# Optimization experiments

Measured on AMD Instinct MI355X. Metric: run time of the kernel, lower is better.

Reference implementation:

```python
import jax, jax.numpy as jnp
import numpy as np

H, C = 4, 32          # heads, per-head channels (hidden=128)
NEG_SLOPE = 0.2        # PyG GATv2Conv default LeakyReLU slope


def setup_inputs() -> dict:
    key = jax.random.key(0)
    ks = jax.random.split(key, 9)
    N_a, N_m = 100000, 50000     # asset / market node counts
    E_aa, E_am = 600000, 400000  # edge counts per edge type
    D, L = 128, 2                # hidden dims, num GAT layers
    sc = 1.0 / np.sqrt(D).astype(np.float32)

    x_asset = jax.random.normal(ks[0], (N_a, D), jnp.float32)
    x_market = jax.random.normal(ks[1], (N_m, D), jnp.float32)

    edge_aa = jax.random.randint(ks[2], (2, E_aa), 0, N_a, jnp.int32)
    src_am = jax.random.randint(ks[3], (E_am,), 0, N_a, jnp.int32)
    dst_am = jax.random.randint(ks[4], (E_am,), 0, N_m, jnp.int32)
    edge_am = jnp.stack([src_am, dst_am])

    Wl = jax.random.normal(ks[5], (L, D, D), jnp.float32) * sc   # lin_l (src)
    Wr = jax.random.normal(ks[6], (L, D, D), jnp.float32) * sc   # lin_r (dst)
    att = jax.random.normal(ks[7], (L, H, C), jnp.float32) * sc  # attention vector
    bias = jnp.zeros((L, D), jnp.float32)

    return {"x_asset": x_asset, "x_market": x_market,
            "edge_aa": edge_aa, "edge_am": edge_am,
            "Wl": Wl, "Wr": Wr, "att": att, "bias": bias}


def _gatv2(x_src, x_dst, src, dst, Wl, Wr, att, bias):
    """One GATv2Conv: gather-attend-scatter. x_src:[Ns,D], x_dst:[Nd,D]."""
    N_dst = x_dst.shape[0]
    xl = (x_src @ Wl).reshape(-1, H, C)   # transformed src (messages)
    xr = (x_dst @ Wr).reshape(-1, H, C)   # transformed dst
    z = jax.nn.leaky_relu(xl[src] + xr[dst], NEG_SLOPE)     # [E,H,C]
    e = jnp.einsum('ehc,hc->eh', z, att)                    # [E,H] scores
    # softmax over incoming edges per destination node
    m = jax.lax.stop_gradient(jax.ops.segment_max(e, dst, num_segments=N_dst))
    w = jnp.exp(e - m[dst])
    s = jax.ops.segment_sum(w, dst, num_segments=N_dst)
    alpha = w / jnp.maximum(s[dst], jnp.float32(1e-16))     # [E,H]
    out = jax.ops.segment_sum(alpha[..., None] * xl[src], dst, num_segments=N_dst)
    return out.reshape(N_dst, H * C) + bias


def reference(x_asset, x_market, edge_aa, edge_am, Wl, Wr, att, bias):
    # Faithful to source: x_dict is never updated between layers, so every
    # layer reads the ORIGINAL features and only the last layer's dict is kept.
    L = Wl.shape[0]
    out_asset = out_market = None
    for l in range(L):
        out_asset = _gatv2(x_asset, x_asset, edge_aa[0], edge_aa[1],
                           Wl[l], Wr[l], att[l], bias[l])
        out_market = _gatv2(x_asset, x_market, edge_am[0], edge_am[1],
                            Wl[l], Wr[l], att[l], bias[l])
    return out_asset, out_market
```

## Files before the change

kernel.cpp:

```cpp
#include <hip/hip_runtime.h>
#include <hip/hip_bf16.h>


#define NEG_SLOPE 0.2f

typedef __attribute__((ext_vector_type(8))) short short8;
typedef __attribute__((ext_vector_type(4))) float floatx4;
typedef __attribute__((ext_vector_type(4))) unsigned short us4;

__device__ inline unsigned short f2bf(float x) {
    union { float f; unsigned u; } v; v.f = x;
    unsigned r = v.u + 0x7FFF + ((v.u >> 16) & 1);
    return (unsigned short)(r >> 16);
}
__device__ inline float bf2f(unsigned short h) {
    union { unsigned u; float f; } v; v.u = (unsigned)h << 16;
    return v.f;
}

__device__ inline void stage_w(const float* __restrict__ W, unsigned char* lds, int t) {
    const int n = t & 127;
    const int kh = t >> 7;
    unsigned short hb[32], lb[32];
#pragma unroll
    for (int i = 0; i < 32; ++i) {
        int k = kh * 32 + i;
        float w = W[(size_t)k * 128 + n];
        unsigned short h = f2bf(w);
        hb[i] = h;
        lb[i] = f2bf(w - bf2f(h));
    }
#pragma unroll
    for (int j = 0; j < 4; ++j) {
        int k = kh * 32 + j * 8;
        int off = ((n * 256 + k * 2) ^ ((n & 7) << 4));
        short8 hv, lv;
#pragma unroll
        for (int i = 0; i < 8; ++i) { hv[i] = (short)hb[j * 8 + i]; lv[i] = (short)lb[j * 8 + i]; }
        *(short8*)(&lds[off]) = hv;
        *(short8*)(&lds[32768 + off]) = lv;
    }
}

__device__ inline void mfma_pass(const unsigned char* lds, const short8* ah,
                                 const short8* al, int lr, int lkb, floatx4* acc) {
#pragma unroll
    for (int ks = 0; ks < 4; ++ks) {
#pragma unroll
        for (int ct = 0; ct < 8; ++ct) {
            int n = ct * 16 + lr;
            int off = ((n * 256 + (ks * 32 + lkb) * 2) ^ ((n & 7) << 4));
            short8 bh = *(const short8*)(&lds[off]);
            short8 bl = *(const short8*)(&lds[32768 + off]);
            acc[ct] = __builtin_amdgcn_mfma_f32_16x16x32_bf16(ah[ks], bh, acc[ct], 0, 0, 0);
            acc[ct] = __builtin_amdgcn_mfma_f32_16x16x32_bf16(al[ks], bh, acc[ct], 0, 0, 0);
            acc[ct] = __builtin_amdgcn_mfma_f32_16x16x32_bf16(ah[ks], bl, acc[ct], 0, 0, 0);
        }
    }
}

__global__ __launch_bounds__(512) void gemm_all(const float* __restrict__ Xa,
                                                const float* __restrict__ Xm,
                                                const float* __restrict__ Wl,
                                                const float* __restrict__ Wr,
                                                unsigned short* __restrict__ XLb,
                                                float* __restrict__ XR,
                                                int Na, int Nm, int nblkA) {
    __shared__ __align__(16) unsigned char lds[65536];

    const int t = threadIdx.x;
    const int wv = t >> 6;
    const int l = t & 63;
    const int lr = l & 15;
    const int lkb = (l >> 4) * 8;
    const bool isA = ((int)blockIdx.x < nblkA);
    const int blk = isA ? blockIdx.x : blockIdx.x - nblkA;
    const float* __restrict__ X = isA ? Xa : Xm;
    const int M = isA ? Na : Nm;
    const int arow = blk * 128 + wv * 16 + lr;

    short8 ah[4], al[4];
    if (arow < M) {
#pragma unroll
        for (int ks = 0; ks < 4; ++ks) {
            const float* xp = X + (size_t)arow * 128 + ks * 32 + lkb;
            float4 f0 = *(const float4*)xp;
            float4 f1 = *(const float4*)(xp + 4);
            float xv[8] = {f0.x, f0.y, f0.z, f0.w, f1.x, f1.y, f1.z, f1.w};
            short8 h, lo;
#pragma unroll
            for (int i = 0; i < 8; ++i) {
                unsigned short hb = f2bf(xv[i]);
                h[i] = (short)hb;
                lo[i] = (short)f2bf(xv[i] - bf2f(hb));
            }
            ah[ks] = h; al[ks] = lo;
        }
    } else {
#pragma unroll
        for (int ks = 0; ks < 4; ++ks) { ah[ks] = (short8)0; al[ks] = (short8)0; }
    }

    const int orow0 = blk * 128 + wv * 16 + (l >> 4) * 4;
    floatx4 acc[8];

    if (isA) {
        stage_w(Wl, lds, t);
        __syncthreads();
#pragma unroll
        for (int ct = 0; ct < 8; ++ct) acc[ct] = (floatx4)0.f;
        mfma_pass(lds, ah, al, lr, lkb, acc);
#pragma unroll
        for (int ct = 0; ct < 8; ++ct) {
            int col = ct * 16 + lr;
#pragma unroll
            for (int r = 0; r < 4; ++r) {
                int orow = orow0 + r;
                if (orow < M) XLb[(size_t)orow * 128 + col] = f2bf(acc[ct][r]);
            }
        }
        __syncthreads();
        stage_w(Wr, lds, t);
        __syncthreads();
#pragma unroll
        for (int ct = 0; ct < 8; ++ct) acc[ct] = (floatx4)0.f;
        mfma_pass(lds, ah, al, lr, lkb, acc);
#pragma unroll
        for (int ct = 0; ct < 8; ++ct) {
            int col = ct * 16 + lr;
#pragma unroll
            for (int r = 0; r < 4; ++r) {
                int orow = orow0 + r;
                if (orow < M) XR[(size_t)orow * 128 + col] = acc[ct][r];
            }
        }
    } else {
        stage_w(Wr, lds, t);
        __syncthreads();
#pragma unroll
        for (int ct = 0; ct < 8; ++ct) acc[ct] = (floatx4)0.f;
        mfma_pass(lds, ah, al, lr, lkb, acc);
        float* __restrict__ XRm = XR + (size_t)Na * 128;
#pragma unroll
        for (int ct = 0; ct < 8; ++ct) {
            int col = ct * 16 + lr;
#pragma unroll
            for (int r = 0; r < 4; ++r) {
                int orow = orow0 + r;
                if (orow < M) XRm[(size_t)orow * 128 + col] = acc[ct][r];
            }
        }
    }
}

__global__ void degcount(const int* __restrict__ aadst, const int* __restrict__ amdst,
                         int* __restrict__ deg, int Eaa, int Eam, int Na) {
    const int nqaa = Eaa >> 2, nqam = Eam >> 2;
    int i = blockIdx.x * 256 + threadIdx.x;
    if (i < nqaa) {
        int4 d = ((const int4*)aadst)[i];
        atomicAdd(&deg[d.x], 1); atomicAdd(&deg[d.y], 1);
        atomicAdd(&deg[d.z], 1); atomicAdd(&deg[d.w], 1);
    } else if (i < nqaa + nqam) {
        int4 d = ((const int4*)amdst)[i - nqaa];
        atomicAdd(&deg[Na + d.x], 1); atomicAdd(&deg[Na + d.y], 1);
        atomicAdd(&deg[Na + d.z], 1); atomicAdd(&deg[Na + d.w], 1);
    } else {
        int k = i - (nqaa + nqam);
        int remaa = Eaa & 3, remam = Eam & 3;
        if (k < remaa) atomicAdd(&deg[aadst[nqaa * 4 + k]], 1);
        else if (k - remaa < remam) atomicAdd(&deg[Na + amdst[nqam * 4 + k - remaa]], 1);
    }
}

__global__ void scan_bsum(const int* __restrict__ deg, int* __restrict__ bsum, int N) {
    __shared__ int sd[256];
    int t = threadIdx.x;
    int base = blockIdx.x * 1024 + t * 4;
    int s = 0;
#pragma unroll
    for (int q = 0; q < 4; ++q) { int idx = base + q; if (idx < N) s += deg[idx]; }
    sd[t] = s; __syncthreads();
    for (int off = 128; off > 0; off >>= 1) {
        if (t < off) sd[t] += sd[t + off];
        __syncthreads();
    }
    if (t == 0) bsum[blockIdx.x] = sd[0];
}

__global__ void scan_partials(int* __restrict__ bsum, int nblk) {
    __shared__ int sd[256];
    int t = threadIdx.x;
    int v = (t < nblk) ? bsum[t] : 0;
    sd[t] = v; __syncthreads();
    for (int off = 1; off < 256; off <<= 1) {
        int x = sd[t];
        if (t >= off) x += sd[t - off];
        __syncthreads(); sd[t] = x; __syncthreads();
    }
    if (t < nblk) bsum[t] = (t == 0) ? 0 : sd[t - 1];
    if (t == 0) bsum[nblk] = sd[255];
}

__global__ void scan_final(const int* __restrict__ deg, const int* __restrict__ bsum,
                           int* __restrict__ row_start, int* __restrict__ fill,
                           int N, int nblk) {
    __shared__ int sd[256];
    int t = threadIdx.x;
    int base = blockIdx.x * 1024 + t * 4;
    int v[4]; int s = 0;
#pragma unroll
    for (int q = 0; q < 4; ++q) { int idx = base + q; v[q] = (idx < N) ? deg[idx] : 0; s += v[q]; }
    sd[t] = s; __syncthreads();
    for (int off = 1; off < 256; off <<= 1) {
        int x = sd[t];
        if (t >= off) x += sd[t - off];
        __syncthreads(); sd[t] = x; __syncthreads();
    }
    int run = bsum[blockIdx.x] + ((t == 0) ? 0 : sd[t - 1]);
#pragma unroll
    for (int q = 0; q < 4; ++q) {
        int idx = base + q;
        if (idx < N) { row_start[idx] = run; fill[idx] = run; }
        run += v[q];
    }
    if (blockIdx.x == 0 && t == 0) row_start[N] = bsum[nblk];
}

__global__ void fillcsr(const int* __restrict__ aasrc, const int* __restrict__ aadst,
                        const int* __restrict__ amsrc, const int* __restrict__ amdst,
                        int* __restrict__ fill, int* __restrict__ csr,
                        int Eaa, int Eam, int Na) {
    const int nqaa = Eaa >> 2, nqam = Eam >> 2;
    int i = blockIdx.x * 256 + threadIdx.x;
    if (i < nqaa) {
        int4 sv = ((const int4*)aasrc)[i];
        int4 dv = ((const int4*)aadst)[i];
        csr[atomicAdd(&fill[dv.x], 1)] = sv.x;
        csr[atomicAdd(&fill[dv.y], 1)] = sv.y;
        csr[atomicAdd(&fill[dv.z], 1)] = sv.z;
        csr[atomicAdd(&fill[dv.w], 1)] = sv.w;
    } else if (i < nqaa + nqam) {
        int4 sv = ((const int4*)amsrc)[i - nqaa];
        int4 dv = ((const int4*)amdst)[i - nqaa];
        csr[atomicAdd(&fill[Na + dv.x], 1)] = sv.x;
        csr[atomicAdd(&fill[Na + dv.y], 1)] = sv.y;
        csr[atomicAdd(&fill[Na + dv.z], 1)] = sv.z;
        csr[atomicAdd(&fill[Na + dv.w], 1)] = sv.w;
    } else {
        int k = i - (nqaa + nqam);
        int remaa = Eaa & 3, remam = Eam & 3;
        if (k < remaa)
            csr[atomicAdd(&fill[aadst[nqaa * 4 + k]], 1)] = aasrc[nqaa * 4 + k];
        else if (k - remaa < remam)
            csr[atomicAdd(&fill[Na + amdst[nqam * 4 + k - remaa]], 1)] = amsrc[nqam * 4 + k - remaa];
    }
}

__global__ __launch_bounds__(256) void gather_gat(const unsigned short* __restrict__ XLb,
                                                  const int* __restrict__ csr,
                                                  const int* __restrict__ row_start,
                                                  const float* __restrict__ att,
                                                  const float* __restrict__ bias,
                                                  float* __restrict__ out,
                                                  int Ntot) {
    int wid = (blockIdx.x * 256 + threadIdx.x) >> 6;
    const int l = threadIdx.x & 63;
    if (wid >= Ntot) return;
    const int half = l >> 5;
    const int q = l & 31;

    const float4 av = *(const float4*)(att + (q >> 3) * 32 + (q & 7) * 4);
    const float4 xr = *(const float4*)(out + (size_t)wid * 128 + q * 4);

    const int beg = row_start[wid];
    const int end = row_start[wid + 1];
    float s = 0.f;
    float4 acc = make_float4(0.f, 0.f, 0.f, 0.f);

#pragma unroll 2
    for (int j = beg; j < end; j += 2) {
        int e = j + half;
        bool act = (e < end);
        int src = csr[act ? e : beg];
        const us4 xlv = *(const us4*)(XLb + (size_t)src * 128 + q * 4);
        float x0 = bf2f(xlv[0]), x1 = bf2f(xlv[1]), x2 = bf2f(xlv[2]), x3 = bf2f(xlv[3]);
        float z0 = x0 + xr.x; z0 = fmaxf(z0, NEG_SLOPE * z0);
        float z1 = x1 + xr.y; z1 = fmaxf(z1, NEG_SLOPE * z1);
        float z2 = x2 + xr.z; z2 = fmaxf(z2, NEG_SLOPE * z2);
        float z3 = x3 + xr.w; z3 = fmaxf(z3, NEG_SLOPE * z3);
        float p = z0 * av.x;
        p = fmaf(z1, av.y, p);
        p = fmaf(z2, av.z, p);
        p = fmaf(z3, av.w, p);
        p += __shfl_xor(p, 1);
        p += __shfl_xor(p, 2);
        p += __shfl_xor(p, 4);
        float w = act ? __expf(p) : 0.f;
        s += w;
        acc.x = fmaf(w, x0, acc.x);
        acc.y = fmaf(w, x1, acc.y);
        acc.z = fmaf(w, x2, acc.z);
        acc.w = fmaf(w, x3, acc.w);
    }
    s += __shfl_xor(s, 32);
    acc.x += __shfl_xor(acc.x, 32);
    acc.y += __shfl_xor(acc.y, 32);
    acc.z += __shfl_xor(acc.z, 32);
    acc.w += __shfl_xor(acc.w, 32);

    if (half == 0) {
        float inv = 1.f / fmaxf(s, 1e-16f);
        const float4 bv = *(const float4*)(bias + q * 4);
        float4 o = make_float4(fmaf(acc.x, inv, bv.x), fmaf(acc.y, inv, bv.y),
                               fmaf(acc.z, inv, bv.z), fmaf(acc.w, inv, bv.w));
        *(float4*)(out + (size_t)wid * 128 + q * 4) = o;
    }
}

extern "C" void kernel_launch(void* const* d_in, const int* in_sizes, int n_in,
                              void* d_out, int out_size, void* d_ws, size_t ws_size,
                              hipStream_t stream) {
    const float* x_asset  = (const float*)d_in[0];
    const float* x_market = (const float*)d_in[1];
    const int*   eaa      = (const int*)d_in[2];
    const int*   eam      = (const int*)d_in[3];
    const float* Wl       = (const float*)d_in[4];
    const float* Wr       = (const float*)d_in[5];
    const float* att      = (const float*)d_in[6];
    const float* bias     = (const float*)d_in[7];

    const int Na  = in_sizes[0] / 128;
    const int Nm  = in_sizes[1] / 128;
    const int Eaa = in_sizes[2] / 2;
    const int Eam = in_sizes[3] / 2;
    const int Ntot = Na + Nm;

    const float* Wl1   = Wl + 128 * 128;
    const float* Wr1   = Wr + 128 * 128;
    const float* att1  = att + 128;
    const float* bias1 = bias + 128;

    unsigned short* XLb = (unsigned short*)d_ws;
    int*   deg = (int*)(XLb + (size_t)Na * 128);
    int*   fill = deg + Ntot;
    int*   bsum = fill + Ntot;
    int*   row_start = bsum + 260;
    int*   csr = row_start + Ntot + 1;

    float* XR = (float*)d_out;

    hipMemsetAsync(deg, 0, sizeof(int) * (size_t)Ntot, stream);

    const int nblkA = (Na + 127) / 128;
    const int nblkM = (Nm + 127) / 128;
    gemm_all<<<nblkA + nblkM, 512, 0, stream>>>(x_asset, x_market, Wl1, Wr1,
                                                XLb, XR, Na, Nm, nblkA);

    const int nq = (Eaa >> 2) + (Eam >> 2) + 8;
    degcount<<<(nq + 255) / 256, 256, 0, stream>>>(eaa + Eaa, eam + Eam, deg, Eaa, Eam, Na);

    const int nblk = (Ntot + 1023) / 1024;
    scan_bsum<<<nblk, 256, 0, stream>>>(deg, bsum, Ntot);
    scan_partials<<<1, 256, 0, stream>>>(bsum, nblk);
    scan_final<<<nblk, 256, 0, stream>>>(deg, bsum, row_start, fill, Ntot, nblk);

    fillcsr<<<(nq + 255) / 256, 256, 0, stream>>>(eaa, eaa + Eaa, eam, eam + Eam,
                                                  fill, csr, Eaa, Eam, Na);

    gather_gat<<<(Ntot * 64 + 255) / 256, 256, 0, stream>>>(
        XLb, csr, row_start, att1, bias1, (float*)d_out, Ntot);
}
```

Measured before the change: 389.5 us.

## Fuse degree count into GEMM, replace scan with atomic segment allocation, unroll gather

Degree counting moves into the GEMM kernel's prologue, and the three-kernel prefix scan is replaced by a single kernel that gives each node an arbitrary contiguous CSR segment through an atomic cursor. The gather loop now processes four edges per half-wave per iteration so more loads are in flight. This cuts several kernel launches and serial scan steps. In exchange, segments are no longer ordered by node, which can hurt locality, and the atomic cursor becomes a contention point.

```diff
diff --git a/kernel.cpp b/kernel.cpp
--- a/kernel.cpp
+++ b/kernel.cpp
@@ -65,7 +65,20 @@
                                                 const float* __restrict__ Wr,
                                                 unsigned short* __restrict__ XLb,
                                                 float* __restrict__ XR,
+                                                const int* __restrict__ aadst,
+                                                const int* __restrict__ amdst,
+                                                int* __restrict__ deg,
+                                                int Eaa, int Eam,
                                                 int Na, int Nm, int nblkA) {
+    {
+        const int stride = gridDim.x * 512;
+        const int E = Eaa + Eam;
+        for (int e = blockIdx.x * 512 + threadIdx.x; e < E; e += stride) {
+            int d = (e < Eaa) ? aadst[e] : (Na + amdst[e - Eaa]);
+            atomicAdd(&deg[d], 1);
+        }
+    }
+
     __shared__ __align__(16) unsigned char lds[65536];
 
     const int t = threadIdx.x;
@@ -153,78 +166,15 @@
     }
 }
 
-__global__ void degcount(const int* __restrict__ aadst, const int* __restrict__ amdst,
-                         int* __restrict__ deg, int Eaa, int Eam, int Na) {
-    const int nqaa = Eaa >> 2, nqam = Eam >> 2;
+__global__ void alloc_seg(const int* __restrict__ deg, int* __restrict__ row_start,
+                          int* __restrict__ fill, int* __restrict__ cursor, int N) {
     int i = blockIdx.x * 256 + threadIdx.x;
-    if (i < nqaa) {
-        int4 d = ((const int4*)aadst)[i];
-        atomicAdd(&deg[d.x], 1); atomicAdd(&deg[d.y], 1);
-        atomicAdd(&deg[d.z], 1); atomicAdd(&deg[d.w], 1);
-    } else if (i < nqaa + nqam) {
-        int4 d = ((const int4*)amdst)[i - nqaa];
-        atomicAdd(&deg[Na + d.x], 1); atomicAdd(&deg[Na + d.y], 1);
-        atomicAdd(&deg[Na + d.z], 1); atomicAdd(&deg[Na + d.w], 1);
-    } else {
-        int k = i - (nqaa + nqam);
-        int remaa = Eaa & 3, remam = Eam & 3;
-        if (k < remaa) atomicAdd(&deg[aadst[nqaa * 4 + k]], 1);
-        else if (k - remaa < remam) atomicAdd(&deg[Na + amdst[nqam * 4 + k - remaa]], 1);
-    }
-}
-
-__global__ void scan_bsum(const int* __restrict__ deg, int* __restrict__ bsum, int N) {
-    __shared__ int sd[256];
-    int t = threadIdx.x;
-    int base = blockIdx.x * 1024 + t * 4;
-    int s = 0;
-#pragma unroll
-    for (int q = 0; q < 4; ++q) { int idx = base + q; if (idx < N) s += deg[idx]; }
-    sd[t] = s; __syncthreads();
-    for (int off = 128; off > 0; off >>= 1) {
-        if (t < off) sd[t] += sd[t + off];
-        __syncthreads();
-    }
-    if (t == 0) bsum[blockIdx.x] = sd[0];
-}
-
-__global__ void scan_partials(int* __restrict__ bsum, int nblk) {
-    __shared__ int sd[256];
-    int t = threadIdx.x;
-    int v = (t < nblk) ? bsum[t] : 0;
-    sd[t] = v; __syncthreads();
-    for (int off = 1; off < 256; off <<= 1) {
-        int x = sd[t];
-        if (t >= off) x += sd[t - off];
-        __syncthreads(); sd[t] = x; __syncthreads();
-    }
-    if (t < nblk) bsum[t] = (t == 0) ? 0 : sd[t - 1];
-    if (t == 0) bsum[nblk] = sd[255];
-}
-
-__global__ void scan_final(const int* __restrict__ deg, const int* __restrict__ bsum,
-                           int* __restrict__ row_start, int* __restrict__ fill,
-                           int N, int nblk) {
-    __shared__ int sd[256];
-    int t = threadIdx.x;
-    int base = blockIdx.x * 1024 + t * 4;
-    int v[4]; int s = 0;
-#pragma unroll
-    for (int q = 0; q < 4; ++q) { int idx = base + q; v[q] = (idx < N) ? deg[idx] : 0; s += v[q]; }
-    sd[t] = s; __syncthreads();
-    for (int off = 1; off < 256; off <<= 1) {
-        int x = sd[t];
-        if (t >= off) x += sd[t - off];
-        __syncthreads(); sd[t] = x; __syncthreads();
-    }
-    int run = bsum[blockIdx.x] + ((t == 0) ? 0 : sd[t - 1]);
-#pragma unroll
-    for (int q = 0; q < 4; ++q) {
-        int idx = base + q;
-        if (idx < N) { row_start[idx] = run; fill[idx] = run; }
-        run += v[q];
-    }
-    if (blockIdx.x == 0 && t == 0) row_start[N] = bsum[nblk];
+    if (i < N) {
+        int d = deg[i];
+        int r = atomicAdd(cursor, d);
+        row_start[i] = r;
+        fill[i] = r;
+    }
 }
 
 __global__ void fillcsr(const int* __restrict__ aasrc, const int* __restrict__ aadst,
@@ -260,6 +210,7 @@
 __global__ __launch_bounds__(256) void gather_gat(const unsigned short* __restrict__ XLb,
                                                   const int* __restrict__ csr,
                                                   const int* __restrict__ row_start,
+                                                  const int* __restrict__ deg,
                                                   const float* __restrict__ att,
                                                   const float* __restrict__ bias,
                                                   float* __restrict__ out,
@@ -274,35 +225,51 @@
     const float4 xr = *(const float4*)(out + (size_t)wid * 128 + q * 4);
 
     const int beg = row_start[wid];
-    const int end = row_start[wid + 1];
+    const int end = beg + deg[wid];
     float s = 0.f;
     float4 acc = make_float4(0.f, 0.f, 0.f, 0.f);
 
-#pragma unroll 2
-    for (int j = beg; j < end; j += 2) {
-        int e = j + half;
-        bool act = (e < end);
-        int src = csr[act ? e : beg];
-        const us4 xlv = *(const us4*)(XLb + (size_t)src * 128 + q * 4);
-        float x0 = bf2f(xlv[0]), x1 = bf2f(xlv[1]), x2 = bf2f(xlv[2]), x3 = bf2f(xlv[3]);
-        float z0 = x0 + xr.x; z0 = fmaxf(z0, NEG_SLOPE * z0);
-        float z1 = x1 + xr.y; z1 = fmaxf(z1, NEG_SLOPE * z1);
-        float z2 = x2 + xr.z; z2 = fmaxf(z2, NEG_SLOPE * z2);
-        float z3 = x3 + xr.w; z3 = fmaxf(z3, NEG_SLOPE * z3);
-        float p = z0 * av.x;
-        p = fmaf(z1, av.y, p);
-        p = fmaf(z2, av.z, p);
-        p = fmaf(z3, av.w, p);
-        p += __shfl_xor(p, 1);
-        p += __shfl_xor(p, 2);
-        p += __shfl_xor(p, 4);
-        float w = act ? __expf(p) : 0.f;
-        s += w;
-        acc.x = fmaf(w, x0, acc.x);
-        acc.y = fmaf(w, x1, acc.y);
-        acc.z = fmaf(w, x2, acc.z);
-        acc.w = fmaf(w, x3, acc.w);
-    }
+#define EDGE(rv, act)                                                        \
+    {                                                                        \
+        float x0 = bf2f(rv[0]), x1 = bf2f(rv[1]), x2 = bf2f(rv[2]), x3 = bf2f(rv[3]); \
+        float z0 = x0 + xr.x; z0 = fmaxf(z0, NEG_SLOPE * z0);                \
+        float z1 = x1 + xr.y; z1 = fmaxf(z1, NEG_SLOPE * z1);                \
+        float z2 = x2 + xr.z; z2 = fmaxf(z2, NEG_SLOPE * z2);                \
+        float z3 = x3 + xr.w; z3 = fmaxf(z3, NEG_SLOPE * z3);                \
+        float p = z0 * av.x;                                                 \
+        p = fmaf(z1, av.y, p);                                               \
+        p = fmaf(z2, av.z, p);                                               \
+        p = fmaf(z3, av.w, p);                                               \
+        p += __shfl_xor(p, 1);                                               \
+        p += __shfl_xor(p, 2);                                               \
+        p += __shfl_xor(p, 4);                                               \
+        float w = (act) ? __expf(p) : 0.f;                                   \
+        s += w;                                                              \
+        acc.x = fmaf(w, x0, acc.x);                                          \
+        acc.y = fmaf(w, x1, acc.y);                                          \
+        acc.z = fmaf(w, x2, acc.z);                                          \
+        acc.w = fmaf(w, x3, acc.w);                                          \
+    }
+
+    for (int j = beg; j < end; j += 8) {
+        const int b = j + half * 4;
+        const bool a0 = (b + 0) < end, a1 = (b + 1) < end,
+                   a2 = (b + 2) < end, a3 = (b + 3) < end;
+        int s0 = csr[a0 ? b + 0 : beg];
+        int s1 = csr[a1 ? b + 1 : beg];
+        int s2 = csr[a2 ? b + 2 : beg];
+        int s3 = csr[a3 ? b + 3 : beg];
+        const us4 r0 = *(const us4*)(XLb + (size_t)s0 * 128 + q * 4);
+        const us4 r1 = *(const us4*)(XLb + (size_t)s1 * 128 + q * 4);
+        const us4 r2 = *(const us4*)(XLb + (size_t)s2 * 128 + q * 4);
+        const us4 r3 = *(const us4*)(XLb + (size_t)s3 * 128 + q * 4);
+        EDGE(r0, a0);
+        EDGE(r1, a1);
+        EDGE(r2, a2);
+        EDGE(r3, a3);
+    }
+#undef EDGE
+
     s += __shfl_xor(s, 32);
     acc.x += __shfl_xor(acc.x, 32);
     acc.y += __shfl_xor(acc.y, 32);
@@ -343,31 +310,27 @@
 
     unsigned short* XLb = (unsigned short*)d_ws;
     int*   deg = (int*)(XLb + (size_t)Na * 128);
-    int*   fill = deg + Ntot;
-    int*   bsum = fill + Ntot;
-    int*   row_start = bsum + 260;
-    int*   csr = row_start + Ntot + 1;
+    int*   cursor = deg + Ntot;
+    int*   fill = cursor + 1;
+    int*   row_start = fill + Ntot;
+    int*   csr = row_start + Ntot;
 
     float* XR = (float*)d_out;
 
-    hipMemsetAsync(deg, 0, sizeof(int) * (size_t)Ntot, stream);
+    hipMemsetAsync(deg, 0, sizeof(int) * (size_t)(Ntot + 1), stream);
 
     const int nblkA = (Na + 127) / 128;
     const int nblkM = (Nm + 127) / 128;
     gemm_all<<<nblkA + nblkM, 512, 0, stream>>>(x_asset, x_market, Wl1, Wr1,
-                                                XLb, XR, Na, Nm, nblkA);
+                                                XLb, XR, eaa + Eaa, eam + Eam,
+                                                deg, Eaa, Eam, Na, Nm, nblkA);
+
+    alloc_seg<<<(Ntot + 255) / 256, 256, 0, stream>>>(deg, row_start, fill, cursor, Ntot);
 
     const int nq = (Eaa >> 2) + (Eam >> 2) + 8;
-    degcount<<<(nq + 255) / 256, 256, 0, stream>>>(eaa + Eaa, eam + Eam, deg, Eaa, Eam, Na);
-
-    const int nblk = (Ntot + 1023) / 1024;
-    scan_bsum<<<nblk, 256, 0, stream>>>(deg, bsum, Ntot);
-    scan_partials<<<1, 256, 0, stream>>>(bsum, nblk);
-    scan_final<<<nblk, 256, 0, stream>>>(deg, bsum, row_start, fill, Ntot, nblk);
-
     fillcsr<<<(nq + 255) / 256, 256, 0, stream>>>(eaa, eaa + Eaa, eam, eam + Eam,
                                                   fill, csr, Eaa, Eam, Na);
 
     gather_gat<<<(Ntot * 64 + 255) / 256, 256, 0, stream>>>(
-        XLb, csr, row_start, att1, bias1, (float*)d_out, Ntot);
-}
+        XLb, csr, row_start, deg, att1, bias1, (float*)d_out, Ntot);
+}
```

Result: faster. 365.7 us (-6.1%).
